# Kernel tuning notes

Hardware: AMD Instinct MI355X
Metric: run time of the kernel (lower is better)

Reference implementation:

```python
import jax, jax.numpy as jnp
import numpy as np

EMBED_DIM = 1024
N_HEADS = 16

def setup_inputs() -> dict:
    key = jax.random.key(0)
    k1, k2, k3 = jax.random.split(key, 3)
    x = jax.random.normal(k1, (4, 2048, EMBED_DIM), dtype=jnp.float32)
    # nn.Linear(D, 3D): store weight as [D, 3D] for x @ W
    W_qkv = jax.random.normal(k2, (EMBED_DIM, 3 * EMBED_DIM), dtype=jnp.float32) * (1.0 / np.sqrt(EMBED_DIM))
    b_qkv = jax.random.normal(k3, (3 * EMBED_DIM,), dtype=jnp.float32) * 0.02
    return {"x": x, "W_qkv": W_qkv, "b_qkv": b_qkv}

def reference(x, W_qkv, b_qkv):
    bs, T, D = x.shape
    nh = N_HEADS
    hs = D // nh
    # fused qkv projection -> [bs, T, nh, 3, hs] (matches view(bs,T,nh,3*hs) + split(hs))
    qkv = (jnp.einsum('btd,de->bte', x, W_qkv) + b_qkv).reshape(bs, T, nh, 3, hs)
    q = qkv[..., 0, :].transpose(0, 2, 1, 3)  # [bs, nh, T, hs]
    k = qkv[..., 1, :].transpose(0, 2, 1, 3)
    v = qkv[..., 2, :].transpose(0, 2, 1, 3)
    scale = 1.0 / np.sqrt(hs).astype(np.float32)
    scores = jnp.einsum('bhqd,bhkd->bhqk', q, k) * scale  # [bs, nh, T, T]
    attn = jax.nn.softmax(scores, axis=-1)
    out = jnp.einsum('bhqk,bhkd->bhqd', attn, v)  # [bs, nh, T, hs]
    return out.transpose(0, 2, 1, 3).reshape(bs, T, D)
```

## Files before the change

kernel.cpp:

```cpp
#include <hip/hip_runtime.h>
#include <stdint.h>

#define T_SEQ 2048
#define DMODEL 1024
#define NHEAD 16
#define HS 64
#define N3 3072
#define BSZ 4
#define MTOT (BSZ*T_SEQ)

typedef __attribute__((ext_vector_type(8))) short bf16x8;
typedef __attribute__((ext_vector_type(4))) float f32x4;
typedef __attribute__((ext_vector_type(16))) float f32x16;
typedef __attribute__((ext_vector_type(2))) unsigned int uint2v;

#define QSCALE 0.18033688011112042f
#define SM_SHIFT 12.0f

#define BH_STRIDE 131072

__device__ inline unsigned short f2bf(float f){
  union { float f; uint32_t u; } v; v.f = f;
  uint32_t r = (v.u + 0x7fffu + ((v.u >> 16) & 1u)) >> 16;
  return (unsigned short)r;
}

__device__ inline uint32_t cvtpk_bf16(float lo, float hi){
  uint32_t r;
  asm("v_cvt_pk_bf16_f32 %0, %1, %2" : "=v"(r) : "v"(lo), "v"(hi));
  return r;
}

__device__ inline void plswap(uint32_t &a, uint32_t &b){
  uint2v r = __builtin_amdgcn_permlane32_swap(a, b, false, false);
  a = r[0]; b = r[1];
}

__device__ inline void gld16(const void* g, void* l){
  __builtin_amdgcn_global_load_lds((const __attribute__((address_space(1))) void*)g,
                                   (__attribute__((address_space(3))) void*)l, 16, 0, 0);
}

__global__ __launch_bounds__(256) void cvt_x(const float* __restrict__ x,
                                             unsigned short* __restrict__ xb, int n){
  int stride = gridDim.x * blockDim.x;
  for (int i = blockIdx.x * blockDim.x + threadIdx.x; i * 4 < n; i += stride){
    const float4 v = *(const float4*)(x + (size_t)i * 4);
    ushort4 o; o.x = f2bf(v.x); o.y = f2bf(v.y); o.z = f2bf(v.z); o.w = f2bf(v.w);
    *(ushort4*)(xb + (size_t)i * 4) = o;
  }
}

__global__ __launch_bounds__(256) void cvt_wt(const float* __restrict__ W,
                                              unsigned short* __restrict__ Wt){
  __shared__ float tile[32][33];
  int bx = blockIdx.x;
  int by = blockIdx.y;
  int tx = threadIdx.x;
  int ty = threadIdx.y;
#pragma unroll
  for (int i = 0; i < 4; i++){
    int k = by * 32 + ty + i * 8;
    int n = bx * 32 + tx;
    tile[ty + i * 8][tx] = W[(size_t)k * N3 + n];
  }
  __syncthreads();
#pragma unroll
  for (int i = 0; i < 4; i++){
    int n = bx * 32 + ty + i * 8;
    int k = by * 32 + tx;
    Wt[(size_t)n * DMODEL + k] = f2bf(tile[tx][ty + i * 8]);
  }
}

#define BM 128
#define BN 128
#define BK 32

__global__ __launch_bounds__(256, 2) void gemm_qkv(
    const unsigned short* __restrict__ xb, const unsigned short* __restrict__ wt,
    const float* __restrict__ bias,
    unsigned short* __restrict__ Qb, unsigned short* __restrict__ Kb,
    unsigned short* __restrict__ Vt)
{
  __shared__ unsigned short Al[BM * BK];
  __shared__ unsigned short Bl[BN * BK];
  const int tid = threadIdx.x;
  const int lane = tid & 63;
  const int w  = tid >> 6;
  const int wm = w >> 1, wn = w & 1;
  const int lr = lane & 15, lg = lane >> 4;
  const int m0 = blockIdx.x * BM;
  const int n0 = blockIdx.y * BN;

  f32x4 acc[4][4] = {};

  const int srow = tid >> 2;
  const int scol = (tid & 3) * 8;
  const unsigned short* ga0 = xb + (size_t)(m0 + srow) * DMODEL + scol;
  const unsigned short* gb0 = wt + (size_t)(n0 + srow) * DMODEL + scol;
  unsigned short* la = &Al[tid * 8];
  unsigned short* lb = &Bl[tid * 8];

  for (int k0 = 0; k0 < DMODEL; k0 += BK){
    gld16(ga0 + k0, la);
    gld16(ga0 + k0 + (size_t)64 * DMODEL, la + 2048);
    gld16(gb0 + k0, lb);
    gld16(gb0 + k0 + (size_t)64 * DMODEL, lb + 2048);
    __syncthreads();
    bf16x8 af[4], bfg[4];
#pragma unroll
    for (int i = 0; i < 4; i++){
      af[i]  = *(const bf16x8*)&Al[(wm * 64 + i * 16 + lr) * BK + lg * 8];
      bfg[i] = *(const bf16x8*)&Bl[(wn * 64 + i * 16 + lr) * BK + lg * 8];
    }
#pragma unroll
    for (int i = 0; i < 4; i++)
#pragma unroll
      for (int j = 0; j < 4; j++)
        acc[i][j] = __builtin_amdgcn_mfma_f32_16x16x32_bf16(af[i], bfg[j], acc[i][j], 0, 0, 0);
    __syncthreads();
  }

#pragma unroll
  for (int i = 0; i < 4; i++){
#pragma unroll
    for (int j = 0; j < 4; j++){
      int gn = n0 + wn * 64 + j * 16 + lr;
      float bv = bias[gn];
      int h = gn / 192;
      int rem = gn - h * 192;
      int which = rem >> 6;
      int d = rem & 63;
#pragma unroll
      for (int r = 0; r < 4; r++){
        int gm = m0 + wm * 64 + i * 16 + lg * 4 + r;
        int b = gm >> 11, t = gm & 2047;
        float val = acc[i][j][r] + bv;
        size_t base = (size_t)(b * NHEAD + h) * BH_STRIDE + (size_t)(t >> 5) * 2048;
        if (which == 0)
          Qb[base + (d >> 4) * 512 + ((d >> 3) & 1) * 256 + (t & 31) * 8 + (d & 7)] = f2bf(val * QSCALE);
        else if (which == 1)
          Kb[base + (d >> 4) * 512 + ((d >> 3) & 1) * 256 + (t & 31) * 8 + (d & 7)] = f2bf(val);
        else {
          int kv = t & 31;
          Vt[base + (d >> 5) * 1024 + (kv >> 4) * 512 + ((kv >> 3) & 1) * 256 + (d & 31) * 8 + (kv & 7)] = f2bf(val);
        }
      }
    }
  }
}

__global__ __launch_bounds__(256, 4) void attn(
    const unsigned short* __restrict__ Qb, const unsigned short* __restrict__ Kb,
    const unsigned short* __restrict__ Vt, float* __restrict__ out)
{
  __shared__ unsigned short Kl[2][2048];
  __shared__ unsigned short Vl[2][2048];
  __shared__ float tl[4][32 * 33];

  int flat = blockIdx.x + (blockIdx.y << 4) + (blockIdx.z << 8);
  int wid = (flat & 7) * 128 + (flat >> 3);
  const int bx = wid & 15;
  const int h  = (wid >> 4) & 15;
  const int b  = wid >> 8;

  const int tid = threadIdx.x;
  const int lane = tid & 63;
  const int w = tid >> 6;
  const int ql = lane & 31;
  const int hi = lane >> 5;
  const int bh = b * NHEAD + h;
  const int q0 = bx * 128 + w * 32;

  const unsigned short* Qf = Qb + (size_t)bh * BH_STRIDE;
  const unsigned short* Kg = Kb + (size_t)bh * BH_STRIDE;
  const unsigned short* Vg = Vt + (size_t)bh * BH_STRIDE;

  bf16x8 qf[4];
#pragma unroll
  for (int c = 0; c < 4; c++)
    qf[c] = *(const bf16x8*)(Qf + (size_t)(q0 >> 5) * 2048 + c * 512 + lane * 8);

  f32x16 cinit;
#pragma unroll
  for (int r = 0; r < 16; r++) cinit[r] = -SM_SHIFT;

  f32x16 acc0 = {}, acc1 = {};
  float lA = 0.f, lB = 0.f, lC = 0.f, lD = 0.f;

  gld16(Kg + tid * 8, &Kl[0][tid * 8]);
  gld16(Vg + tid * 8, &Vl[0][tid * 8]);
  __syncthreads();

  for (int t = 0; t < 64; ++t){
    const int cur = t & 1;
    if (t < 63){
      gld16(Kg + (size_t)(t + 1) * 2048 + tid * 8, &Kl[cur ^ 1][tid * 8]);
      gld16(Vg + (size_t)(t + 1) * 2048 + tid * 8, &Vl[cur ^ 1][tid * 8]);
    }

    bf16x8 kf[4], vf[4];
#pragma unroll
    for (int c = 0; c < 4; c++) kf[c] = *(const bf16x8*)&Kl[cur][c * 512 + lane * 8];
#pragma unroll
    for (int c = 0; c < 4; c++) vf[c] = *(const bf16x8*)&Vl[cur][c * 512 + lane * 8];

    f32x16 s = __builtin_amdgcn_mfma_f32_32x32x16_bf16(kf[0], qf[0], cinit, 0, 0, 0);
    s = __builtin_amdgcn_mfma_f32_32x32x16_bf16(kf[1], qf[1], s, 0, 0, 0);
    s = __builtin_amdgcn_mfma_f32_32x32x16_bf16(kf[2], qf[2], s, 0, 0, 0);
    s = __builtin_amdgcn_mfma_f32_32x32x16_bf16(kf[3], qf[3], s, 0, 0, 0);

    uint32_t c8[8];
#pragma unroll
    for (int i = 0; i < 8; i += 2){
      float p0 = __builtin_amdgcn_exp2f(s[2 * i]);
      float p1 = __builtin_amdgcn_exp2f(s[2 * i + 1]);
      float p2 = __builtin_amdgcn_exp2f(s[2 * i + 2]);
      float p3 = __builtin_amdgcn_exp2f(s[2 * i + 3]);
      lA += p0; lB += p1; lC += p2; lD += p3;
      c8[i]     = cvtpk_bf16(p0, p1);
      c8[i + 1] = cvtpk_bf16(p2, p3);
    }
    plswap(c8[0], c8[2]); plswap(c8[1], c8[3]);
    plswap(c8[4], c8[6]); plswap(c8[5], c8[7]);
    union { uint32_t u[4]; bf16x8 v; } pf1, pf2;
    pf1.u[0] = c8[0]; pf1.u[1] = c8[1]; pf1.u[2] = c8[2]; pf1.u[3] = c8[3];
    pf2.u[0] = c8[4]; pf2.u[1] = c8[5]; pf2.u[2] = c8[6]; pf2.u[3] = c8[7];
    acc0 = __builtin_amdgcn_mfma_f32_32x32x16_bf16(vf[0], pf1.v, acc0, 0, 0, 0);
    acc0 = __builtin_amdgcn_mfma_f32_32x32x16_bf16(vf[1], pf2.v, acc0, 0, 0, 0);
    acc1 = __builtin_amdgcn_mfma_f32_32x32x16_bf16(vf[2], pf1.v, acc1, 0, 0, 0);
    acc1 = __builtin_amdgcn_mfma_f32_32x32x16_bf16(vf[3], pf2.v, acc1, 0, 0, 0);

    __syncthreads();
  }

  float l_ = (lA + lB) + (lC + lD);
  l_ += __shfl_xor(l_, 32);
  float inv = 1.0f / l_;

  float* tw = &tl[w][0];
#pragma unroll
  for (int t2 = 0; t2 < 2; t2++){
    const f32x16& A = t2 ? acc1 : acc0;
#pragma unroll
    for (int r = 0; r < 16; r++){
      int dp = (r & 3) + 8 * (r >> 2) + 4 * hi;
      tw[dp * 33 + ql] = A[r] * inv;
    }
    asm volatile("s_waitcnt lgkmcnt(0)" ::: "memory");
    const int cq = lane >> 3;
    const int cc = (lane & 7) * 4;
#pragma unroll
    for (int it = 0; it < 4; it++){
      int q = it * 8 + cq;
      float4 o;
      o.x = tw[(cc + 0) * 33 + q];
      o.y = tw[(cc + 1) * 33 + q];
      o.z = tw[(cc + 2) * 33 + q];
      o.w = tw[(cc + 3) * 33 + q];
      *(float4*)(out + ((size_t)(b * T_SEQ + q0 + q)) * DMODEL + h * HS + t2 * 32 + cc) = o;
    }
    asm volatile("s_waitcnt lgkmcnt(0)" ::: "memory");
  }
}

extern "C" void kernel_launch(void* const* d_in, const int* in_sizes, int n_in,
                              void* d_out, int out_size, void* d_ws, size_t ws_size,
                              hipStream_t stream) {
  const float* x  = (const float*)d_in[0];
  const float* Wq = (const float*)d_in[1];
  const float* bq = (const float*)d_in[2];
  float* out = (float*)d_out;
  uint8_t* ws = (uint8_t*)d_ws;

  unsigned short* xb = (unsigned short*)(ws);
  unsigned short* wt = (unsigned short*)(ws + (size_t)16 * 1024 * 1024);
  unsigned short* Qb = (unsigned short*)(ws + (size_t)22 * 1024 * 1024);
  unsigned short* Kb = (unsigned short*)(ws + (size_t)38 * 1024 * 1024);
  unsigned short* Vt = (unsigned short*)(ws + (size_t)54 * 1024 * 1024);

  cvt_x<<<2048, 256, 0, stream>>>(x, xb, MTOT * DMODEL);
  cvt_wt<<<dim3(N3 / 32, DMODEL / 32), dim3(32, 8), 0, stream>>>(Wq, wt);
  gemm_qkv<<<dim3(MTOT / BM, N3 / BN), 256, 0, stream>>>(xb, wt, bq, Qb, Kb, Vt);
  attn<<<dim3(T_SEQ / 128, NHEAD, BSZ), 256, 0, stream>>>(Qb, Kb, Vt, out);
}
```

Measured before the change: 169.5 us.

## Process two 32-key K/V tiles per iteration with setprio around MFMA chains

The attention loop now loads two 32-key K and V tiles per stage, 64 keys in all, into a double-buffered LDS array. This halves the number of barriers and loop iterations. Both QK^T MFMA chains are issued before either softmax/PV step, so exp and pack work can overlap MFMA latency. s_setprio is raised around each MFMA group to favour matrix issue across waves. The output transpose buffer now reuses the K/V LDS space, which keeps total LDS about the same; this is safe only because the loop ends with a barrier.

Result: slower. 427.2 us (+152.1%).

```diff
diff --git a/kernel.cpp b/kernel.cpp
--- a/kernel.cpp
+++ b/kernel.cpp
@@ -155,9 +155,7 @@
     const unsigned short* __restrict__ Qb, const unsigned short* __restrict__ Kb,
     const unsigned short* __restrict__ Vt, float* __restrict__ out)
 {
-  __shared__ unsigned short Kl[2][2048];
-  __shared__ unsigned short Vl[2][2048];
-  __shared__ float tl[4][32 * 33];
+  __shared__ unsigned short KVs[2][2][2][2048];
 
   int flat = blockIdx.x + (blockIdx.y << 4) + (blockIdx.z << 8);
   int wid = (flat & 7) * 128 + (flat >> 3);
@@ -189,57 +187,94 @@
   f32x16 acc0 = {}, acc1 = {};
   float lA = 0.f, lB = 0.f, lC = 0.f, lD = 0.f;
 
-  gld16(Kg + tid * 8, &Kl[0][tid * 8]);
-  gld16(Vg + tid * 8, &Vl[0][tid * 8]);
+  gld16(Kg +        tid * 8, &KVs[0][0][0][tid * 8]);
+  gld16(Kg + 2048 + tid * 8, &KVs[0][0][1][tid * 8]);
+  gld16(Vg +        tid * 8, &KVs[0][1][0][tid * 8]);
+  gld16(Vg + 2048 + tid * 8, &KVs[0][1][1][tid * 8]);
   __syncthreads();
 
-  for (int t = 0; t < 64; ++t){
+#define SOFTMAX_PACK(S, PF1, PF2) \
+    uint32_t c8[8]; \
+    _Pragma("unroll") \
+    for (int i = 0; i < 8; i += 2){ \
+      float p0 = __builtin_amdgcn_exp2f((S)[2 * i]); \
+      float p1 = __builtin_amdgcn_exp2f((S)[2 * i + 1]); \
+      float p2 = __builtin_amdgcn_exp2f((S)[2 * i + 2]); \
+      float p3 = __builtin_amdgcn_exp2f((S)[2 * i + 3]); \
+      lA += p0; lB += p1; lC += p2; lD += p3; \
+      c8[i]     = cvtpk_bf16(p0, p1); \
+      c8[i + 1] = cvtpk_bf16(p2, p3); \
+    } \
+    plswap(c8[0], c8[2]); plswap(c8[1], c8[3]); \
+    plswap(c8[4], c8[6]); plswap(c8[5], c8[7]); \
+    PF1.u[0] = c8[0]; PF1.u[1] = c8[1]; PF1.u[2] = c8[2]; PF1.u[3] = c8[3]; \
+    PF2.u[0] = c8[4]; PF2.u[1] = c8[5]; PF2.u[2] = c8[6]; PF2.u[3] = c8[7];
+
+  for (int t = 0; t < 32; ++t){
     const int cur = t & 1;
-    if (t < 63){
-      gld16(Kg + (size_t)(t + 1) * 2048 + tid * 8, &Kl[cur ^ 1][tid * 8]);
-      gld16(Vg + (size_t)(t + 1) * 2048 + tid * 8, &Vl[cur ^ 1][tid * 8]);
-    }
-
-    bf16x8 kf[4], vf[4];
-#pragma unroll
-    for (int c = 0; c < 4; c++) kf[c] = *(const bf16x8*)&Kl[cur][c * 512 + lane * 8];
-#pragma unroll
-    for (int c = 0; c < 4; c++) vf[c] = *(const bf16x8*)&Vl[cur][c * 512 + lane * 8];
-
-    f32x16 s = __builtin_amdgcn_mfma_f32_32x32x16_bf16(kf[0], qf[0], cinit, 0, 0, 0);
-    s = __builtin_amdgcn_mfma_f32_32x32x16_bf16(kf[1], qf[1], s, 0, 0, 0);
-    s = __builtin_amdgcn_mfma_f32_32x32x16_bf16(kf[2], qf[2], s, 0, 0, 0);
-    s = __builtin_amdgcn_mfma_f32_32x32x16_bf16(kf[3], qf[3], s, 0, 0, 0);
-
-    uint32_t c8[8];
-#pragma unroll
-    for (int i = 0; i < 8; i += 2){
-      float p0 = __builtin_amdgcn_exp2f(s[2 * i]);
-      float p1 = __builtin_amdgcn_exp2f(s[2 * i + 1]);
-      float p2 = __builtin_amdgcn_exp2f(s[2 * i + 2]);
-      float p3 = __builtin_amdgcn_exp2f(s[2 * i + 3]);
-      lA += p0; lB += p1; lC += p2; lD += p3;
-      c8[i]     = cvtpk_bf16(p0, p1);
-      c8[i + 1] = cvtpk_bf16(p2, p3);
-    }
-    plswap(c8[0], c8[2]); plswap(c8[1], c8[3]);
-    plswap(c8[4], c8[6]); plswap(c8[5], c8[7]);
-    union { uint32_t u[4]; bf16x8 v; } pf1, pf2;
-    pf1.u[0] = c8[0]; pf1.u[1] = c8[1]; pf1.u[2] = c8[2]; pf1.u[3] = c8[3];
-    pf2.u[0] = c8[4]; pf2.u[1] = c8[5]; pf2.u[2] = c8[6]; pf2.u[3] = c8[7];
-    acc0 = __builtin_amdgcn_mfma_f32_32x32x16_bf16(vf[0], pf1.v, acc0, 0, 0, 0);
-    acc0 = __builtin_amdgcn_mfma_f32_32x32x16_bf16(vf[1], pf2.v, acc0, 0, 0, 0);
-    acc1 = __builtin_amdgcn_mfma_f32_32x32x16_bf16(vf[2], pf1.v, acc1, 0, 0, 0);
-    acc1 = __builtin_amdgcn_mfma_f32_32x32x16_bf16(vf[3], pf2.v, acc1, 0, 0, 0);
+    if (t < 31){
+      const size_t g0 = (size_t)(2 * t + 2) * 2048 + tid * 8;
+      gld16(Kg + g0,        &KVs[cur ^ 1][0][0][tid * 8]);
+      gld16(Kg + g0 + 2048, &KVs[cur ^ 1][0][1][tid * 8]);
+      gld16(Vg + g0,        &KVs[cur ^ 1][1][0][tid * 8]);
+      gld16(Vg + g0 + 2048, &KVs[cur ^ 1][1][1][tid * 8]);
+    }
+
+    bf16x8 kfA[4], vfA[4];
+#pragma unroll
+    for (int c = 0; c < 4; c++) kfA[c] = *(const bf16x8*)&KVs[cur][0][0][c * 512 + lane * 8];
+#pragma unroll
+    for (int c = 0; c < 4; c++) vfA[c] = *(const bf16x8*)&KVs[cur][1][0][c * 512 + lane * 8];
+    __builtin_amdgcn_s_setprio(1);
+    f32x16 sA = __builtin_amdgcn_mfma_f32_32x32x16_bf16(kfA[0], qf[0], cinit, 0, 0, 0);
+    sA = __builtin_amdgcn_mfma_f32_32x32x16_bf16(kfA[1], qf[1], sA, 0, 0, 0);
+    sA = __builtin_amdgcn_mfma_f32_32x32x16_bf16(kfA[2], qf[2], sA, 0, 0, 0);
+    sA = __builtin_amdgcn_mfma_f32_32x32x16_bf16(kfA[3], qf[3], sA, 0, 0, 0);
+    __builtin_amdgcn_s_setprio(0);
+
+    bf16x8 kfB[4], vfB[4];
+#pragma unroll
+    for (int c = 0; c < 4; c++) kfB[c] = *(const bf16x8*)&KVs[cur][0][1][c * 512 + lane * 8];
+#pragma unroll
+    for (int c = 0; c < 4; c++) vfB[c] = *(const bf16x8*)&KVs[cur][1][1][c * 512 + lane * 8];
+    __builtin_amdgcn_s_setprio(1);
+    f32x16 sB = __builtin_amdgcn_mfma_f32_32x32x16_bf16(kfB[0], qf[0], cinit, 0, 0, 0);
+    sB = __builtin_amdgcn_mfma_f32_32x32x16_bf16(kfB[1], qf[1], sB, 0, 0, 0);
+    sB = __builtin_amdgcn_mfma_f32_32x32x16_bf16(kfB[2], qf[2], sB, 0, 0, 0);
+    sB = __builtin_amdgcn_mfma_f32_32x32x16_bf16(kfB[3], qf[3], sB, 0, 0, 0);
+    __builtin_amdgcn_s_setprio(0);
+
+    {
+      union { uint32_t u[4]; bf16x8 v; } pf1, pf2;
+      SOFTMAX_PACK(sA, pf1, pf2)
+      __builtin_amdgcn_s_setprio(1);
+      acc0 = __builtin_amdgcn_mfma_f32_32x32x16_bf16(vfA[0], pf1.v, acc0, 0, 0, 0);
+      acc0 = __builtin_amdgcn_mfma_f32_32x32x16_bf16(vfA[1], pf2.v, acc0, 0, 0, 0);
+      acc1 = __builtin_amdgcn_mfma_f32_32x32x16_bf16(vfA[2], pf1.v, acc1, 0, 0, 0);
+      acc1 = __builtin_amdgcn_mfma_f32_32x32x16_bf16(vfA[3], pf2.v, acc1, 0, 0, 0);
+      __builtin_amdgcn_s_setprio(0);
+    }
+    {
+      union { uint32_t u[4]; bf16x8 v; } pf1, pf2;
+      SOFTMAX_PACK(sB, pf1, pf2)
+      __builtin_amdgcn_s_setprio(1);
+      acc0 = __builtin_amdgcn_mfma_f32_32x32x16_bf16(vfB[0], pf1.v, acc0, 0, 0, 0);
+      acc0 = __builtin_amdgcn_mfma_f32_32x32x16_bf16(vfB[1], pf2.v, acc0, 0, 0, 0);
+      acc1 = __builtin_amdgcn_mfma_f32_32x32x16_bf16(vfB[2], pf1.v, acc1, 0, 0, 0);
+      acc1 = __builtin_amdgcn_mfma_f32_32x32x16_bf16(vfB[3], pf2.v, acc1, 0, 0, 0);
+      __builtin_amdgcn_s_setprio(0);
+    }
 
     __syncthreads();
   }
+#undef SOFTMAX_PACK
 
   float l_ = (lA + lB) + (lC + lD);
   l_ += __shfl_xor(l_, 32);
   float inv = 1.0f / l_;
 
-  float* tw = &tl[w][0];
+  float* tl = (float*)&KVs[0][0][0][0];
+  float* tw = tl + w * (32 * 33);
 #pragma unroll
   for (int t2 = 0; t2 < 2; t2++){
     const f32x16& A = t2 ? acc1 : acc0;
```
